# Kernel optimization log

Measured on AMD Instinct MI355X. Metric: run time of the kernel, lower is better.

Reference implementation:

```python
import jax, jax.numpy as jnp
import numpy as np

B, S, H, R = 4, 1024, 1024, 32


def setup_inputs() -> dict:
    key = jax.random.key(0)
    k1, k2, k3 = jax.random.split(key, 3)
    hidden_states = jax.random.normal(k1, (B, S, H), dtype=jnp.float32)
    # full cartesian grid of (seq_idx, hidden_idx), as required by the final
    # out.view(B, S, H, 1) reshape in the original module
    n = jnp.arange(S * H, dtype=jnp.int64)
    all_indices = jnp.stack([n // H, n % H], axis=1)  # [S*H, 2]
    # Linear weights, torch layout [out_features, in_features], scaled like kaiming-uniform-ish
    seq_W = jax.random.normal(k2, (R, H), dtype=jnp.float32) / np.sqrt(H)
    hid_W = jax.random.normal(k3, (R, S), dtype=jnp.float32) / np.sqrt(S)
    cp_weight = jnp.ones((1, R), dtype=jnp.float32)  # frozen all-ones CP mixing weight
    return {"hidden_states": hidden_states, "all_indices": all_indices,
            "seq_W": seq_W, "hid_W": hid_W, "cp_weight": cp_weight}


def reference(hidden_states, all_indices, seq_W, hid_W, cp_weight):
    # seq-mode factor: Linear(H -> R) over [B, S, H] -> [B, S, R]
    seq_emb = jnp.einsum('bsh,rh->bsr', hidden_states, seq_W)
    # hidden-mode factor: Linear(S -> R) over transposed [B, H, S] -> [B, H, R]
    hid_emb = jnp.einsum('bsh,rs->bhr', hidden_states, hid_W)
    s_idx = all_indices[:, 0]  # [N]
    h_idx = all_indices[:, 1]  # [N]
    g_seq = seq_emb[:, s_idx, :]  # [B, N, R] gather along seq axis
    g_hid = hid_emb[:, h_idx, :]  # [B, N, R] gather along hidden axis
    # hadamard + rank reduction with (frozen) CP weight; out_units == 1 squeezed
    out = jnp.einsum('bnr,bnr,r->bn', g_seq, g_hid, cp_weight[0])
    return out.reshape(B, S, H)
```

## Files before the change

kernel.cpp:

```cpp
#include <hip/hip_runtime.h>

typedef __attribute__((ext_vector_type(8))) short bf16x8;
typedef __attribute__((ext_vector_type(4))) float f32x4;
typedef __attribute__((ext_vector_type(2))) float f32x2;

__device__ __forceinline__ short f2bf(float x) {
    union { __bf16 h; short s; } u;
    u.h = (__bf16)x;
    return u.s;
}

__global__ __launch_bounds__(256) void gemm_fused(
    const float* __restrict__ hs, const float* __restrict__ seqW,
    const float* __restrict__ hidW, float* __restrict__ E )
{
    __shared__ float red[4][16][32];

    const int bid = blockIdx.x;
    const bool hid = bid >= 256;
    const int mt  = hid ? bid - 256 : bid;
    const int tid = threadIdx.x;
    const int wv  = tid >> 6;
    const int l   = tid & 63;
    const int l15 = l & 15;
    const int g   = l >> 4;
    const int m0  = mt * 16;
    const int mrow = m0 + l15;

    const float* __restrict__ W = hid ? hidW : seqW;
    size_t arow;
    if (hid) arow = ((size_t)(mrow >> 10) << 20) + (size_t)(mrow & 1023);
    else     arow = (size_t)mrow << 10;

    f32x4 acc0 = {0.f,0.f,0.f,0.f}, acc1 = {0.f,0.f,0.f,0.f};
    const int kbase = wv * 256;

    for (int ks = 0; ks < 8; ++ks) {
        const int kb = kbase + ks * 32 + g * 8;
        bf16x8 af, bf0, bf1;
        if (hid) {
            const float* pa = hs + arow + (size_t)kb * 1024;
            float a[8];
            #pragma unroll
            for (int j = 0; j < 8; ++j) a[j] = pa[(size_t)j * 1024];
            #pragma unroll
            for (int j = 0; j < 8; ++j) af[j] = f2bf(a[j]);
        } else {
            const f32x4* pa = (const f32x4*)(hs + arow + kb);
            f32x4 a0 = pa[0], a1 = pa[1];
            af[0]=f2bf(a0.x); af[1]=f2bf(a0.y); af[2]=f2bf(a0.z); af[3]=f2bf(a0.w);
            af[4]=f2bf(a1.x); af[5]=f2bf(a1.y); af[6]=f2bf(a1.z); af[7]=f2bf(a1.w);
        }
        {
            const f32x4* pb = (const f32x4*)(W + (size_t)l15 * 1024 + kb);
            f32x4 b0 = pb[0], b1 = pb[1];
            bf0[0]=f2bf(b0.x); bf0[1]=f2bf(b0.y); bf0[2]=f2bf(b0.z); bf0[3]=f2bf(b0.w);
            bf0[4]=f2bf(b1.x); bf0[5]=f2bf(b1.y); bf0[6]=f2bf(b1.z); bf0[7]=f2bf(b1.w);
        }
        {
            const f32x4* pb = (const f32x4*)(W + (size_t)(l15 + 16) * 1024 + kb);
            f32x4 b0 = pb[0], b1 = pb[1];
            bf1[0]=f2bf(b0.x); bf1[1]=f2bf(b0.y); bf1[2]=f2bf(b0.z); bf1[3]=f2bf(b0.w);
            bf1[4]=f2bf(b1.x); bf1[5]=f2bf(b1.y); bf1[6]=f2bf(b1.z); bf1[7]=f2bf(b1.w);
        }
        acc0 = __builtin_amdgcn_mfma_f32_16x16x32_bf16(af, bf0, acc0, 0, 0, 0);
        acc1 = __builtin_amdgcn_mfma_f32_16x16x32_bf16(af, bf1, acc1, 0, 0, 0);
    }

    #pragma unroll
    for (int r = 0; r < 4; ++r) {
        red[wv][4 * g + r][l15]      = acc0[r];
        red[wv][4 * g + r][l15 + 16] = acc1[r];
    }
    __syncthreads();

    const int o = tid * 2;
    const float* rf = &red[0][0][0];
    f32x2 v;
    v.x = rf[o]     + rf[512 + o]     + rf[1024 + o]     + rf[1536 + o];
    v.y = rf[o + 1] + rf[512 + o + 1] + rf[1024 + o + 1] + rf[1536 + o + 1];
    float* Eo = E + (hid ? (size_t)4096 * 32 : 0) + (size_t)m0 * 32 + o;
    *(f32x2*)Eo = v;
}

__global__ __launch_bounds__(256) void k3(const float* __restrict__ SeqE,
                                          const float* __restrict__ HidE,
                                          const float* __restrict__ cpw,
                                          float* __restrict__ out)
{
    __shared__ float s_w[32][36];
    __shared__ float s_h[64][36];
    const int tid = threadIdx.x;
    const int b  = blockIdx.z;
    const int s0 = blockIdx.x * 32;
    const int h0 = blockIdx.y * 64;

    {
        const int si = tid >> 3;
        const int r4 = (tid & 7) * 4;
        f32x4 v  = *(const f32x4*)(SeqE + ((size_t)(b * 1024 + s0 + si)) * 32 + r4);
        f32x4 wv = *(const f32x4*)(cpw + r4);
        v *= wv;
        *(f32x4*)&s_w[si][r4] = v;
    }
    #pragma unroll
    for (int t = 0; t < 2; ++t) {
        const int fi = tid + t * 256;
        const int hx = fi >> 3;
        const int r4 = (fi & 7) * 4;
        f32x4 v = *(const f32x4*)(HidE + ((size_t)(b * 1024 + h0 + hx)) * 32 + r4);
        *(f32x4*)&s_h[hx][r4] = v;
    }
    __syncthreads();

    const int hx = tid & 63;
    const int sg = tid >> 6;
    float hv[32];
    #pragma unroll
    for (int r4 = 0; r4 < 32; r4 += 4) {
        f32x4 v = *(const f32x4*)&s_h[hx][r4];
        hv[r4] = v.x; hv[r4+1] = v.y; hv[r4+2] = v.z; hv[r4+3] = v.w;
    }
    float res[8];
    #pragma unroll
    for (int si = 0; si < 8; ++si) {
        const int s = sg * 8 + si;
        float acc = 0.f;
        #pragma unroll
        for (int r4 = 0; r4 < 32; r4 += 4) {
            f32x4 v = *(const f32x4*)&s_w[s][r4];
            acc += v.x * hv[r4] + v.y * hv[r4+1] + v.z * hv[r4+2] + v.w * hv[r4+3];
        }
        res[si] = acc;
    }
    #pragma unroll
    for (int si = 0; si < 8; ++si) {
        const int s = s0 + sg * 8 + si;
        out[((size_t)(b * 1024 + s)) * 1024 + h0 + hx] = res[si];
    }
}

extern "C" void kernel_launch(void* const* d_in, const int* in_sizes, int n_in,
                              void* d_out, int out_size, void* d_ws, size_t ws_size,
                              hipStream_t stream) {
    const float* hs   = (const float*)d_in[0];
    const float* seqW = (const float*)d_in[2];
    const float* hidW = (const float*)d_in[3];
    const float* cpw  = (const float*)d_in[4];
    float* out = (float*)d_out;

    float* E = (float*)d_ws;

    gemm_fused<<<512, 256, 0, stream>>>(hs, seqW, hidW, E);
    dim3 grid3(32, 16, 4);
    k3<<<grid3, 256, 0, stream>>>(E, E + (size_t)4096 * 32, cpw, out);
}
```

Measured before the change: 25.22 us.

## Fold CP weight into GEMM epilogue and drop LDS staging in outer-product kernel

The GEMM kernel now runs 512-thread blocks that each cover 32 rows, with two row sub-tiles and four K slices, halving the grid, and it multiplies the seq embeddings by the CP weight in its epilogue. The outer-product kernel drops its shared-memory staging and barrier: each thread keeps its hidden-row embedding in registers and reads seq rows directly from global memory, relying on uniform addresses being served by cache. This removes LDS traffic and a sync from k3 and the cp-weight work from it, at the cost of more global/scalar loads and fewer, larger GEMM blocks.

Result: slower. 30.76 us (+22.0%).

```diff
diff --git a/kernel.cpp b/kernel.cpp
--- a/kernel.cpp
+++ b/kernel.cpp
@@ -10,22 +10,25 @@
     return u.s;
 }
 
-__global__ __launch_bounds__(256) void gemm_fused(
+__global__ __launch_bounds__(512) void gemm_fused(
     const float* __restrict__ hs, const float* __restrict__ seqW,
-    const float* __restrict__ hidW, float* __restrict__ E )
+    const float* __restrict__ hidW, const float* __restrict__ cpw,
+    float* __restrict__ E )
 {
-    __shared__ float red[4][16][32];
+    __shared__ float red[8][16][32];
 
     const int bid = blockIdx.x;
-    const bool hid = bid >= 256;
-    const int mt  = hid ? bid - 256 : bid;
+    const bool hid = bid >= 128;
+    const int mt  = hid ? bid - 128 : bid;
     const int tid = threadIdx.x;
     const int wv  = tid >> 6;
+    const int sub = wv & 1;
+    const int kslice = wv >> 1;
     const int l   = tid & 63;
     const int l15 = l & 15;
     const int g   = l >> 4;
-    const int m0  = mt * 16;
-    const int mrow = m0 + l15;
+    const int m0  = mt * 32;
+    const int mrow = m0 + sub * 16 + l15;
 
     const float* __restrict__ W = hid ? hidW : seqW;
     size_t arow;
@@ -33,7 +36,7 @@
     else     arow = (size_t)mrow << 10;
 
     f32x4 acc0 = {0.f,0.f,0.f,0.f}, acc1 = {0.f,0.f,0.f,0.f};
-    const int kbase = wv * 256;
+    const int kbase = kslice * 256;
 
     for (int ks = 0; ks < 8; ++ks) {
         const int kb = kbase + ks * 32 + g * 8;
@@ -74,69 +77,50 @@
     }
     __syncthreads();
 
-    const int o = tid * 2;
+    const int o    = tid * 2;
+    const int subo = o >> 9;
+    const int idx  = o & 511;
     const float* rf = &red[0][0][0];
     f32x2 v;
-    v.x = rf[o]     + rf[512 + o]     + rf[1024 + o]     + rf[1536 + o];
-    v.y = rf[o + 1] + rf[512 + o + 1] + rf[1024 + o + 1] + rf[1536 + o + 1];
+    v.x = rf[subo * 512 + idx]        + rf[(subo + 2) * 512 + idx]
+        + rf[(subo + 4) * 512 + idx]  + rf[(subo + 6) * 512 + idx];
+    v.y = rf[subo * 512 + idx + 1]       + rf[(subo + 2) * 512 + idx + 1]
+        + rf[(subo + 4) * 512 + idx + 1] + rf[(subo + 6) * 512 + idx + 1];
+    if (!hid) {
+        f32x2 w = *(const f32x2*)(cpw + (o & 31));
+        v.x *= w.x; v.y *= w.y;
+    }
     float* Eo = E + (hid ? (size_t)4096 * 32 : 0) + (size_t)m0 * 32 + o;
     *(f32x2*)Eo = v;
 }
 
 __global__ __launch_bounds__(256) void k3(const float* __restrict__ SeqE,
                                           const float* __restrict__ HidE,
-                                          const float* __restrict__ cpw,
                                           float* __restrict__ out)
 {
-    __shared__ float s_w[32][36];
-    __shared__ float s_h[64][36];
     const int tid = threadIdx.x;
     const int b  = blockIdx.z;
     const int s0 = blockIdx.x * 32;
     const int h0 = blockIdx.y * 64;
+    const int hx = tid & 63;
+    const int sg = __builtin_amdgcn_readfirstlane(tid >> 6);
 
-    {
-        const int si = tid >> 3;
-        const int r4 = (tid & 7) * 4;
-        f32x4 v  = *(const f32x4*)(SeqE + ((size_t)(b * 1024 + s0 + si)) * 32 + r4);
-        f32x4 wv = *(const f32x4*)(cpw + r4);
-        v *= wv;
-        *(f32x4*)&s_w[si][r4] = v;
-    }
+    const f32x4* hrow = (const f32x4*)(HidE + ((size_t)(b * 1024 + h0 + hx)) * 32);
+    f32x4 hv[8];
     #pragma unroll
-    for (int t = 0; t < 2; ++t) {
-        const int fi = tid + t * 256;
-        const int hx = fi >> 3;
-        const int r4 = (fi & 7) * 4;
-        f32x4 v = *(const f32x4*)(HidE + ((size_t)(b * 1024 + h0 + hx)) * 32 + r4);
-        *(f32x4*)&s_h[hx][r4] = v;
-    }
-    __syncthreads();
+    for (int i = 0; i < 8; ++i) hv[i] = hrow[i];
 
-    const int hx = tid & 63;
-    const int sg = tid >> 6;
-    float hv[32];
-    #pragma unroll
-    for (int r4 = 0; r4 < 32; r4 += 4) {
-        f32x4 v = *(const f32x4*)&s_h[hx][r4];
-        hv[r4] = v.x; hv[r4+1] = v.y; hv[r4+2] = v.z; hv[r4+3] = v.w;
-    }
-    float res[8];
-    #pragma unroll
-    for (int si = 0; si < 8; ++si) {
-        const int s = sg * 8 + si;
-        float acc = 0.f;
-        #pragma unroll
-        for (int r4 = 0; r4 < 32; r4 += 4) {
-            f32x4 v = *(const f32x4*)&s_w[s][r4];
-            acc += v.x * hv[r4] + v.y * hv[r4+1] + v.z * hv[r4+2] + v.w * hv[r4+3];
-        }
-        res[si] = acc;
-    }
     #pragma unroll
     for (int si = 0; si < 8; ++si) {
         const int s = s0 + sg * 8 + si;
-        out[((size_t)(b * 1024 + s)) * 1024 + h0 + hx] = res[si];
+        const f32x4* wrow = (const f32x4*)(SeqE + ((size_t)(b * 1024 + s)) * 32);
+        float acc = 0.f;
+        #pragma unroll
+        for (int r4 = 0; r4 < 8; ++r4) {
+            f32x4 w = wrow[r4];
+            acc += w.x * hv[r4].x + w.y * hv[r4].y + w.z * hv[r4].z + w.w * hv[r4].w;
+        }
+        out[((size_t)(b * 1024 + s)) * 1024 + h0 + hx] = acc;
     }
 }
 
@@ -151,7 +135,7 @@
 
     float* E = (float*)d_ws;
 
-    gemm_fused<<<512, 256, 0, stream>>>(hs, seqW, hidW, E);
+    gemm_fused<<<256, 512, 0, stream>>>(hs, seqW, hidW, cpw, E);
     dim3 grid3(32, 16, 4);
-    k3<<<grid3, 256, 0, stream>>>(E, E + (size_t)4096 * 32, cpw, out);
+    k3<<<grid3, 256, 0, stream>>>(E, E + (size_t)4096 * 32, out);
 }
```

## Stage hidden-mode GEMM tiles through LDS with split-K partials and reduce kernel

Applied to the files above, without the earlier changes.

The hidden-mode projection previously read hidden_states with a stride of 1024 floats per element, giving uncoalesced scalar loads. Blocks now load coalesced 64x64 tiles of hidden_states into LDS and read transposed bf16 fragments from there. Each block covers a 256-long slice of the sequence dimension and writes partial sums to a workspace buffer. A new small kernel then adds the four partials. This adds one kernel launch and extra workspace traffic.

Result: slower. 27.72 us (+9.9%).

```diff
diff --git a/kernel.cpp b/kernel.cpp
--- a/kernel.cpp
+++ b/kernel.cpp
@@ -12,75 +12,122 @@
 
 __global__ __launch_bounds__(256) void gemm_fused(
     const float* __restrict__ hs, const float* __restrict__ seqW,
-    const float* __restrict__ hidW, float* __restrict__ E )
+    const float* __restrict__ hidW, float* __restrict__ E ,
+    float* __restrict__ P )
 {
-    __shared__ float red[4][16][32];
+    __shared__ float lds[64 * 68];
 
     const int bid = blockIdx.x;
-    const bool hid = bid >= 256;
-    const int mt  = hid ? bid - 256 : bid;
     const int tid = threadIdx.x;
     const int wv  = tid >> 6;
     const int l   = tid & 63;
     const int l15 = l & 15;
     const int g   = l >> 4;
-    const int m0  = mt * 16;
-    const int mrow = m0 + l15;
-
-    const float* __restrict__ W = hid ? hidW : seqW;
-    size_t arow;
-    if (hid) arow = ((size_t)(mrow >> 10) << 20) + (size_t)(mrow & 1023);
-    else     arow = (size_t)mrow << 10;
-
-    f32x4 acc0 = {0.f,0.f,0.f,0.f}, acc1 = {0.f,0.f,0.f,0.f};
-    const int kbase = wv * 256;
-
-    for (int ks = 0; ks < 8; ++ks) {
-        const int kb = kbase + ks * 32 + g * 8;
-        bf16x8 af, bf0, bf1;
-        if (hid) {
-            const float* pa = hs + arow + (size_t)kb * 1024;
-            float a[8];
+
+    if (bid < 256) {
+        const int m0 = bid * 16;
+        const size_t arow = (size_t)(m0 + l15) << 10;
+        f32x4 acc0 = {0.f,0.f,0.f,0.f}, acc1 = {0.f,0.f,0.f,0.f};
+        const int kbase = wv * 256;
+
+        for (int ks = 0; ks < 8; ++ks) {
+            const int kb = kbase + ks * 32 + g * 8;
+            bf16x8 af, bf0, bf1;
+            {
+                const f32x4* pa = (const f32x4*)(hs + arow + kb);
+                f32x4 a0 = pa[0], a1 = pa[1];
+                af[0]=f2bf(a0.x); af[1]=f2bf(a0.y); af[2]=f2bf(a0.z); af[3]=f2bf(a0.w);
+                af[4]=f2bf(a1.x); af[5]=f2bf(a1.y); af[6]=f2bf(a1.z); af[7]=f2bf(a1.w);
+            }
+            {
+                const f32x4* pb = (const f32x4*)(seqW + (size_t)l15 * 1024 + kb);
+                f32x4 b0 = pb[0], b1 = pb[1];
+                bf0[0]=f2bf(b0.x); bf0[1]=f2bf(b0.y); bf0[2]=f2bf(b0.z); bf0[3]=f2bf(b0.w);
+                bf0[4]=f2bf(b1.x); bf0[5]=f2bf(b1.y); bf0[6]=f2bf(b1.z); bf0[7]=f2bf(b1.w);
+            }
+            {
+                const f32x4* pb = (const f32x4*)(seqW + (size_t)(l15 + 16) * 1024 + kb);
+                f32x4 b0 = pb[0], b1 = pb[1];
+                bf1[0]=f2bf(b0.x); bf1[1]=f2bf(b0.y); bf1[2]=f2bf(b0.z); bf1[3]=f2bf(b0.w);
+                bf1[4]=f2bf(b1.x); bf1[5]=f2bf(b1.y); bf1[6]=f2bf(b1.z); bf1[7]=f2bf(b1.w);
+            }
+            acc0 = __builtin_amdgcn_mfma_f32_16x16x32_bf16(af, bf0, acc0, 0, 0, 0);
+            acc1 = __builtin_amdgcn_mfma_f32_16x16x32_bf16(af, bf1, acc1, 0, 0, 0);
+        }
+        #pragma unroll
+        for (int r = 0; r < 4; ++r) {
+            lds[wv * 512 + (4 * g + r) * 32 + l15]      = acc0[r];
+            lds[wv * 512 + (4 * g + r) * 32 + l15 + 16] = acc1[r];
+        }
+        __syncthreads();
+        const int o = tid * 2;
+        f32x2 v;
+        v.x = lds[o]     + lds[512 + o]     + lds[1024 + o]     + lds[1536 + o];
+        v.y = lds[o + 1] + lds[512 + o + 1] + lds[1024 + o + 1] + lds[1536 + o + 1];
+        *(f32x2*)(E + (size_t)m0 * 32 + o) = v;
+    } else {
+        const int hb = bid - 256;
+        const int c  = hb & 3;
+        const int t  = hb >> 2;
+        const int b  = t >> 4;
+        const int h0 = (t & 15) * 64;
+        const size_t hsb = (size_t)b << 20;
+
+        f32x4 acc0 = {0.f,0.f,0.f,0.f}, acc1 = {0.f,0.f,0.f,0.f};
+
+        for (int st = 0; st < 4; ++st) {
+            const int s0 = c * 256 + st * 64;
+            __syncthreads();
             #pragma unroll
-            for (int j = 0; j < 8; ++j) a[j] = pa[(size_t)j * 1024];
+            for (int k = 0; k < 4; ++k) {
+                const int flat = tid + k * 256;
+                const int row  = flat >> 4;
+                const int c4   = (flat & 15) * 4;
+                f32x4 vv = *(const f32x4*)(hs + hsb + (size_t)(s0 + row) * 1024 + h0 + c4);
+                *(f32x4*)&lds[row * 68 + c4] = vv;
+            }
+            __syncthreads();
+
             #pragma unroll
-            for (int j = 0; j < 8; ++j) af[j] = f2bf(a[j]);
-        } else {
-            const f32x4* pa = (const f32x4*)(hs + arow + kb);
-            f32x4 a0 = pa[0], a1 = pa[1];
-            af[0]=f2bf(a0.x); af[1]=f2bf(a0.y); af[2]=f2bf(a0.z); af[3]=f2bf(a0.w);
-            af[4]=f2bf(a1.x); af[5]=f2bf(a1.y); af[6]=f2bf(a1.z); af[7]=f2bf(a1.w);
-        }
-        {
-            const f32x4* pb = (const f32x4*)(W + (size_t)l15 * 1024 + kb);
-            f32x4 b0 = pb[0], b1 = pb[1];
-            bf0[0]=f2bf(b0.x); bf0[1]=f2bf(b0.y); bf0[2]=f2bf(b0.z); bf0[3]=f2bf(b0.w);
-            bf0[4]=f2bf(b1.x); bf0[5]=f2bf(b1.y); bf0[6]=f2bf(b1.z); bf0[7]=f2bf(b1.w);
-        }
-        {
-            const f32x4* pb = (const f32x4*)(W + (size_t)(l15 + 16) * 1024 + kb);
-            f32x4 b0 = pb[0], b1 = pb[1];
-            bf1[0]=f2bf(b0.x); bf1[1]=f2bf(b0.y); bf1[2]=f2bf(b0.z); bf1[3]=f2bf(b0.w);
-            bf1[4]=f2bf(b1.x); bf1[5]=f2bf(b1.y); bf1[6]=f2bf(b1.z); bf1[7]=f2bf(b1.w);
-        }
-        acc0 = __builtin_amdgcn_mfma_f32_16x16x32_bf16(af, bf0, acc0, 0, 0, 0);
-        acc1 = __builtin_amdgcn_mfma_f32_16x16x32_bf16(af, bf1, acc1, 0, 0, 0);
-    }
-
-    #pragma unroll
-    for (int r = 0; r < 4; ++r) {
-        red[wv][4 * g + r][l15]      = acc0[r];
-        red[wv][4 * g + r][l15 + 16] = acc1[r];
-    }
-    __syncthreads();
-
-    const int o = tid * 2;
-    const float* rf = &red[0][0][0];
-    f32x2 v;
-    v.x = rf[o]     + rf[512 + o]     + rf[1024 + o]     + rf[1536 + o];
-    v.y = rf[o + 1] + rf[512 + o + 1] + rf[1024 + o + 1] + rf[1536 + o + 1];
-    float* Eo = E + (hid ? (size_t)4096 * 32 : 0) + (size_t)m0 * 32 + o;
-    *(f32x2*)Eo = v;
+            for (int kbl = 0; kbl < 64; kbl += 32) {
+                bf16x8 af, bf0, bf1;
+                #pragma unroll
+                for (int j = 0; j < 8; ++j)
+                    af[j] = f2bf(lds[(kbl + g * 8 + j) * 68 + wv * 16 + l15]);
+                const int kg = c * 256 + st * 64 + kbl + g * 8;
+                {
+                    const f32x4* pb = (const f32x4*)(hidW + (size_t)l15 * 1024 + kg);
+                    f32x4 b0 = pb[0], b1 = pb[1];
+                    bf0[0]=f2bf(b0.x); bf0[1]=f2bf(b0.y); bf0[2]=f2bf(b0.z); bf0[3]=f2bf(b0.w);
+                    bf0[4]=f2bf(b1.x); bf0[5]=f2bf(b1.y); bf0[6]=f2bf(b1.z); bf0[7]=f2bf(b1.w);
+                }
+                {
+                    const f32x4* pb = (const f32x4*)(hidW + (size_t)(l15 + 16) * 1024 + kg);
+                    f32x4 b0 = pb[0], b1 = pb[1];
+                    bf1[0]=f2bf(b0.x); bf1[1]=f2bf(b0.y); bf1[2]=f2bf(b0.z); bf1[3]=f2bf(b0.w);
+                    bf1[4]=f2bf(b1.x); bf1[5]=f2bf(b1.y); bf1[6]=f2bf(b1.z); bf1[7]=f2bf(b1.w);
+                }
+                acc0 = __builtin_amdgcn_mfma_f32_16x16x32_bf16(af, bf0, acc0, 0, 0, 0);
+                acc1 = __builtin_amdgcn_mfma_f32_16x16x32_bf16(af, bf1, acc1, 0, 0, 0);
+            }
+        }
+        float* Pc = P + (size_t)c * 131072;
+        #pragma unroll
+        for (int r = 0; r < 4; ++r) {
+            const int hrow = b * 1024 + h0 + wv * 16 + 4 * g + r;
+            Pc[(size_t)hrow * 32 + l15]      = acc0[r];
+            Pc[(size_t)hrow * 32 + 16 + l15] = acc1[r];
+        }
+    }
+}
+
+__global__ __launch_bounds__(256) void kreduce(const float* __restrict__ P,
+                                               float* __restrict__ Ehid)
+{
+    const int idx = blockIdx.x * 256 + threadIdx.x;
+    const f32x4* P4 = (const f32x4*)P;
+    f32x4 v = P4[idx] + P4[idx + 32768] + P4[idx + 65536] + P4[idx + 98304];
+    ((f32x4*)Ehid)[idx] = v;
 }
 
 __global__ __launch_bounds__(256) void k3(const float* __restrict__ SeqE,
@@ -150,8 +197,10 @@
     float* out = (float*)d_out;
 
     float* E = (float*)d_ws;
-
-    gemm_fused<<<512, 256, 0, stream>>>(hs, seqW, hidW, E);
+    float* P = E + (size_t)2 * 4096 * 32;
+
+    gemm_fused<<<512, 256, 0, stream>>>(hs, seqW, hidW, E, P);
+    kreduce<<<128, 256, 0, stream>>>(P, E + (size_t)4096 * 32);
     dim3 grid3(32, 16, 4);
     k3<<<grid3, 256, 0, stream>>>(E, E + (size_t)4096 * 32, cpw, out);
 }
```
